# Kernel tuning notes

Hardware: AMD Instinct MI355X
Metric: run time of the kernel (lower is better)

Reference implementation:

```python
import jax, jax.numpy as jnp
import numpy as np

N = 50000          # num nodes
E = 1_000_000      # num edges (no self loops by construction)
IN_CH = 128        # in_channels
HEADS = 4
OUT_CH = 16        # out_channels per head
HID = HEADS * OUT_CH  # 64
NEG_SLOPE = 0.2


def setup_inputs() -> dict:
    key = jax.random.key(0)
    k1, k2, k3, k4, k5, k6 = jax.random.split(key, 6)
    x = jax.random.normal(k1, (N, IN_CH), jnp.float32)
    # edges with guaranteed row != col (so add_self_loops == plain concat)
    row = jax.random.randint(k2, (E,), 0, N, dtype=jnp.int32)
    off = jax.random.randint(k3, (E,), 1, N, dtype=jnp.int32)
    col = (row + off) % N
    edge_index = jnp.stack([row, col], axis=0)  # [2, E]
    # xavier-uniform linear weight [HID, IN_CH] (bias=False in module)
    lim_w = float(np.sqrt(6.0 / (IN_CH + HID)))
    W = jax.random.uniform(k4, (HID, IN_CH), jnp.float32, -lim_w, lim_w)
    # xavier-uniform attention vectors [HEADS, OUT_CH]
    lim_a = float(np.sqrt(6.0 / (HEADS + OUT_CH)))
    att_src = jax.random.uniform(k5, (HEADS, OUT_CH), jnp.float32, -lim_a, lim_a)
    att_dst = jax.random.uniform(k6, (HEADS, OUT_CH), jnp.float32, -lim_a, lim_a)
    bias = jnp.zeros((HID,), jnp.float32)
    return {"x": x, "edge_index": edge_index, "W": W,
            "att_src": att_src, "att_dst": att_dst, "bias": bias}


def reference(x, edge_index, W, att_src, att_dst, bias):
    # add self loops (input edges have no self loops, so this matches torch)
    loops = jnp.arange(N, dtype=edge_index.dtype)
    ei = jnp.concatenate([edge_index, jnp.stack([loops, loops], axis=0)], axis=1)
    row, col = ei[0], ei[1]                      # [E+N]
    proj = (x @ W.T).reshape(N, HEADS, OUT_CH)   # [N, H, C]
    src = proj[row]                              # [E+N, H, C] gather
    dst = proj[col]                              # [E+N, H, C] gather
    # MX attention logits per edge per head
    logits = (jnp.einsum('ehc,hc->eh', src, att_src)
              + jnp.einsum('ehc,hc->eh', dst, att_dst))
    logits = jax.nn.leaky_relu(logits, NEG_SLOPE)            # [E+N, H]
    # segment softmax over destination node (all heads at once)
    m = jax.ops.segment_max(logits, col, num_segments=N)    # [N, H]
    e = jnp.exp(logits - m[col])
    s = jax.ops.segment_sum(e, col, num_segments=N)         # [N, H]
    w = e / s[col]                                           # [E+N, H]
    # attention-weighted scatter-add aggregation
    out = jax.ops.segment_sum(src * w[..., None], col, num_segments=N)  # [N, H, C]
    return out.reshape(N, HID) + bias
```

## Files before the change

### kernel.cpp

```cpp
#include <hip/hip_runtime.h>

#define IN_CH   128
#define HEADS   4
#define OUT_CH  16
#define HID     64
#define NEG_SLOPE 0.2f
#define LOG2E   1.44269504088896340736f

#define LDA 136

#define RB      6
#define RSZ     64
#define NRANGE  1024
#define SEG     4096
#define RWIN    2048
#define CWIN    2048

typedef __attribute__((ext_vector_type(8))) short short8;
typedef __attribute__((ext_vector_type(4))) float float4v;

__device__ __forceinline__ unsigned short f2bf(float f) {
    unsigned int u = __float_as_uint(f);
    u += 0x7FFFu + ((u >> 16) & 1u);
    return (unsigned short)(u >> 16);
}
__device__ __forceinline__ float bf2f(unsigned short u) {
    return __uint_as_float(((unsigned int)u) << 16);
}
__device__ __forceinline__ void unpack2(unsigned int u, float& lo, float& hi) {
    lo = __uint_as_float(u << 16);
    hi = __uint_as_float(u & 0xffff0000u);
}

__global__ __launch_bounds__(256) void proj_kernel(
    const float* __restrict__ x,
    const float* __restrict__ W,
    const float* __restrict__ att_src,
    const float* __restrict__ att_dst,
    unsigned short* __restrict__ proj,
    float* __restrict__ asrc,
    float* __restrict__ adst,
    int* __restrict__ gcur,
    int n_nodes)
{
    __shared__ unsigned short As[64 * LDA];
    __shared__ unsigned short Bs[64 * LDA];

    const int tid = threadIdx.x;

    if (blockIdx.x == 0) {
        #pragma unroll
        for (int i = tid; i < NRANGE; i += 256) gcur[i] = i * RWIN;
    }

    const int n0 = blockIdx.x * 64;

    #pragma unroll
    for (int i = 0; i < 8; ++i) {
        int idx4 = i * 256 + tid;
        int row  = idx4 >> 5;
        int c4   = (idx4 & 31) * 4;
        float4 v = *(const float4*)(W + row * IN_CH + c4);
        ushort4 o;
        o.x = f2bf(v.x); o.y = f2bf(v.y); o.z = f2bf(v.z); o.w = f2bf(v.w);
        *(ushort4*)(&Bs[row * LDA + c4]) = o;
    }
    #pragma unroll
    for (int i = 0; i < 8; ++i) {
        int idx4 = i * 256 + tid;
        int row  = idx4 >> 5;
        int c4   = (idx4 & 31) * 4;
        int n    = n0 + row;
        float4 v = make_float4(0.f, 0.f, 0.f, 0.f);
        if (n < n_nodes) v = *(const float4*)(x + (size_t)n * IN_CH + c4);
        ushort4 o;
        o.x = f2bf(v.x); o.y = f2bf(v.y); o.z = f2bf(v.z); o.w = f2bf(v.w);
        *(ushort4*)(&As[row * LDA + c4]) = o;
    }
    __syncthreads();

    const int w    = tid >> 6;
    const int lane = tid & 63;
    const int l16  = lane & 15;
    const int quad = lane >> 4;

    float4v acc0 = {0.f,0.f,0.f,0.f};
    float4v acc1 = {0.f,0.f,0.f,0.f};
    float4v acc2 = {0.f,0.f,0.f,0.f};
    float4v acc3 = {0.f,0.f,0.f,0.f};

    const unsigned short* arow = &As[(w * 16 + l16) * LDA + quad * 8];
    const unsigned short* b0   = &Bs[( 0 + l16) * LDA + quad * 8];
    const unsigned short* b1   = &Bs[(16 + l16) * LDA + quad * 8];
    const unsigned short* b2   = &Bs[(32 + l16) * LDA + quad * 8];
    const unsigned short* b3   = &Bs[(48 + l16) * LDA + quad * 8];

    #pragma unroll
    for (int k0 = 0; k0 < IN_CH; k0 += 32) {
        short8 a  = *(const short8*)(arow + k0);
        acc0 = __builtin_amdgcn_mfma_f32_16x16x32_bf16(a, *(const short8*)(b0 + k0), acc0, 0, 0, 0);
        acc1 = __builtin_amdgcn_mfma_f32_16x16x32_bf16(a, *(const short8*)(b1 + k0), acc1, 0, 0, 0);
        acc2 = __builtin_amdgcn_mfma_f32_16x16x32_bf16(a, *(const short8*)(b2 + k0), acc2, 0, 0, 0);
        acc3 = __builtin_amdgcn_mfma_f32_16x16x32_bf16(a, *(const short8*)(b3 + k0), acc3, 0, 0, 0);
    }

    const float as0 = att_src[ 0 + l16], ad0 = att_dst[ 0 + l16];
    const float as1 = att_src[16 + l16], ad1 = att_dst[16 + l16];
    const float as2 = att_src[32 + l16], ad2 = att_dst[32 + l16];
    const float as3 = att_src[48 + l16], ad3 = att_dst[48 + l16];

    #pragma unroll
    for (int r = 0; r < 4; ++r) {
        const int n = n0 + w * 16 + quad * 4 + r;
        const bool ok = (n < n_nodes);
        float v0 = acc0[r], v1 = acc1[r], v2 = acc2[r], v3 = acc3[r];
        if (ok) {
            proj[(size_t)n * HID +  0 + l16] = f2bf(v0);
            proj[(size_t)n * HID + 16 + l16] = f2bf(v1);
            proj[(size_t)n * HID + 32 + l16] = f2bf(v2);
            proj[(size_t)n * HID + 48 + l16] = f2bf(v3);
        }
        float s0 = v0 * as0, s1 = v1 * as1, s2 = v2 * as2, s3 = v3 * as3;
        float d0 = v0 * ad0, d1 = v1 * ad1, d2 = v2 * ad2, d3 = v3 * ad3;
        #pragma unroll
        for (int off = 8; off >= 1; off >>= 1) {
            s0 += __shfl_down(s0, off, 16);
            s1 += __shfl_down(s1, off, 16);
            s2 += __shfl_down(s2, off, 16);
            s3 += __shfl_down(s3, off, 16);
            d0 += __shfl_down(d0, off, 16);
            d1 += __shfl_down(d1, off, 16);
            d2 += __shfl_down(d2, off, 16);
            d3 += __shfl_down(d3, off, 16);
        }
        if (ok && l16 == 0) {
            asrc[n * HEADS + 0] = s0 * LOG2E;
            asrc[n * HEADS + 1] = s1 * LOG2E;
            asrc[n * HEADS + 2] = s2 * LOG2E;
            asrc[n * HEADS + 3] = s3 * LOG2E;
            adst[n * HEADS + 0] = d0 * LOG2E;
            adst[n * HEADS + 1] = d1 * LOG2E;
            adst[n * HEADS + 2] = d2 * LOG2E;
            adst[n * HEADS + 3] = d3 * LOG2E;
        }
    }
}

__global__ __launch_bounds__(256) void bin_kernel(
    const int* __restrict__ src, const int* __restrict__ dst,
    int* __restrict__ gcur, unsigned int* __restrict__ ebuf, int n_edges)
{
    __shared__ unsigned int eb[SEG];
    __shared__ int lc[NRANGE];

    const int b = blockIdx.x;
    const int t = threadIdx.x;

    #pragma unroll
    for (int i = t; i < NRANGE; i += 256) lc[i] = 0;
    __syncthreads();

    const int e0  = b * SEG;
    const int e1  = min(e0 + SEG, n_edges);
    const int cnt = e1 - e0;

    for (int e = e0 + t * 4; e < e1; e += 1024) {
        if (e + 4 <= e1) {
            const int4 s4 = *(const int4*)(src + e);
            const int4 d4 = *(const int4*)(dst + e);
            {
                const int r = d4.x >> RB; atomicAdd(&lc[r], 1);
                eb[e - e0 + 0] = ((unsigned int)r << 22) | ((unsigned int)(d4.x & (RSZ - 1)) << 16) | (unsigned int)s4.x;
            }
            {
                const int r = d4.y >> RB; atomicAdd(&lc[r], 1);
                eb[e - e0 + 1] = ((unsigned int)r << 22) | ((unsigned int)(d4.y & (RSZ - 1)) << 16) | (unsigned int)s4.y;
            }
            {
                const int r = d4.z >> RB; atomicAdd(&lc[r], 1);
                eb[e - e0 + 2] = ((unsigned int)r << 22) | ((unsigned int)(d4.z & (RSZ - 1)) << 16) | (unsigned int)s4.z;
            }
            {
                const int r = d4.w >> RB; atomicAdd(&lc[r], 1);
                eb[e - e0 + 3] = ((unsigned int)r << 22) | ((unsigned int)(d4.w & (RSZ - 1)) << 16) | (unsigned int)s4.w;
            }
        } else {
            for (int q = e; q < e1; ++q) {
                const int d = dst[q];
                const int r = d >> RB;
                atomicAdd(&lc[r], 1);
                eb[q - e0] = ((unsigned int)r << 22) | ((unsigned int)(d & (RSZ - 1)) << 16) | (unsigned int)src[q];
            }
        }
    }
    __syncthreads();

    for (int r = t; r < NRANGE; r += 256) {
        const int c = lc[r];
        lc[r] = c ? atomicAdd(&gcur[r], c) : 0;
    }
    __syncthreads();

    for (int j = t; j < cnt; j += 256) {
        const unsigned int p = eb[j];
        const int slot = atomicAdd(&lc[p >> 22], 1);
        ebuf[slot] = p & 0x3FFFFFu;
    }
}

__global__ __launch_bounds__(256) void range_csr_kernel(
    const unsigned int* __restrict__ ebuf, const int* __restrict__ gcur,
    int2* __restrict__ rsdeg, unsigned short* __restrict__ csr, int n_nodes)
{
    __shared__ int hist[RSZ];
    __shared__ int cur[RSZ];

    const int r    = blockIdx.x;
    const int base = r << RB;
    const int lim  = min(RSZ, n_nodes - base);
    const int tid  = threadIdx.x;

    const int s0 = r * RWIN;
    const int s1 = gcur[r];

    if (tid < RSZ) hist[tid] = 0;
    __syncthreads();

    for (int j = s0 + tid; j < s1; j += 256)
        atomicAdd(&hist[ebuf[j] >> 16], 1);
    __syncthreads();

    if (tid < RSZ) {
        const int hv = hist[tid];
        int hc = hv;
        #pragma unroll
        for (int o = 1; o < 64; o <<= 1) {
            int u = __shfl_up(hc, o);
            if (tid >= o) hc += u;
        }
        const int start = r * CWIN + hc - hv;
        cur[tid] = start;
        if (tid < lim) rsdeg[base + tid] = make_int2(start, hv);
    }
    __syncthreads();

    for (int j = s0 + tid; j < s1; j += 256) {
        const unsigned int p = ebuf[j];
        const int slot = atomicAdd(&cur[p >> 16], 1);
        csr[slot] = (unsigned short)p;
    }
}

__global__ __launch_bounds__(256) void gather_kernel(
    const unsigned short* __restrict__ proj,
    const float* __restrict__ asrc,
    const float* __restrict__ adst,
    const int2* __restrict__ rsdeg,
    const unsigned short* __restrict__ csr,
    const float* __restrict__ bias,
    float* __restrict__ out,
    int n_nodes, int chunk)
{
    const int nb = (blockIdx.x & 7) * chunk + (blockIdx.x >> 3);
    const int l  = threadIdx.x & 63;
    const int w  = threadIdx.x >> 6;
    const int il = l & 7;
    const int g  = l >> 3;
    const int h  = il >> 1;
    const int ch = il * 8;

    int n = nb * 32 + w * 8 + g;
    const bool nok = (n < n_nodes);
    if (!nok) n = 0;

    const float  ad  = adst[n * HEADS + h];
    const float4 bv0 = *(const float4*)(bias + ch);
    const float4 bv1 = *(const float4*)(bias + ch + 4);

    float zs = asrc[n * HEADS + h] + ad;
    zs = fmaxf(zs, NEG_SLOPE * zs);
    float s = exp2f(zs);
    float a0, a1, a2, a3, a4, a5, a6, a7;
    {
        const uint4 ps = *(const uint4*)(proj + (size_t)n * HID + ch);
        float p0, p1, p2, p3, p4, p5, p6, p7;
        unpack2(ps.x, p0, p1); unpack2(ps.y, p2, p3);
        unpack2(ps.z, p4, p5); unpack2(ps.w, p6, p7);
        a0 = s * p0; a1 = s * p1; a2 = s * p2; a3 = s * p3;
        a4 = s * p4; a5 = s * p5; a6 = s * p6; a7 = s * p7;
    }

    const int2 rd   = rsdeg[n];
    const int start = rd.x;
    const int deg   = nok ? rd.y : 0;

    int m = deg;
    m = max(m, __shfl_xor(m, 8));
    m = max(m, __shfl_xor(m, 16));
    m = max(m, __shfl_xor(m, 32));
    const int kmax = __builtin_amdgcn_readfirstlane(m);

    #define STEP(K)                                                           \
    {                                                                         \
        const bool act = (K) < deg;                                           \
        int sid = (int)csr[start + (K)];   \
        sid = act ? sid : 0;                  \
        const uint4 pv = *(const uint4*)(proj + (size_t)sid * HID + ch);      \
        float av = asrc[sid * HEADS + h] + ad;                                \
        av = fmaxf(av, NEG_SLOPE * av);                                       \
        float e = exp2f(av);                                                  \
        e = act ? e : 0.f;                                                    \
        s += e;                                                               \
        float p0, p1, p2, p3, p4, p5, p6, p7;                                 \
        unpack2(pv.x, p0, p1); unpack2(pv.y, p2, p3);                         \
        unpack2(pv.z, p4, p5); unpack2(pv.w, p6, p7);                         \
        a0 = fmaf(e, p0, a0); a1 = fmaf(e, p1, a1);                           \
        a2 = fmaf(e, p2, a2); a3 = fmaf(e, p3, a3);                           \
        a4 = fmaf(e, p4, a4); a5 = fmaf(e, p5, a5);                           \
        a6 = fmaf(e, p6, a6); a7 = fmaf(e, p7, a7);                           \
    }

    for (int k = 0; k < kmax; k += 4) {
        STEP(k);
        STEP(k + 1);
        STEP(k + 2);
        STEP(k + 3);
    }
    #undef STEP

    if (nok) {
        const float inv = 1.0f / s;
        float4 o0, o1;
        o0.x = a0 * inv + bv0.x;
        o0.y = a1 * inv + bv0.y;
        o0.z = a2 * inv + bv0.z;
        o0.w = a3 * inv + bv0.w;
        o1.x = a4 * inv + bv1.x;
        o1.y = a5 * inv + bv1.y;
        o1.z = a6 * inv + bv1.z;
        o1.w = a7 * inv + bv1.w;
        *(float4*)(out + (size_t)n * HID + ch)     = o0;
        *(float4*)(out + (size_t)n * HID + ch + 4) = o1;
    }
}

static inline size_t align16(size_t o) { return (o + 15) & ~(size_t)15; }

extern "C" void kernel_launch(void* const* d_in, const int* in_sizes, int n_in,
                              void* d_out, int out_size, void* d_ws, size_t ws_size,
                              hipStream_t stream)
{
    const float* x       = (const float*)d_in[0];
    const int*   ei      = (const int*)d_in[1];
    const float* W       = (const float*)d_in[2];
    const float* att_src = (const float*)d_in[3];
    const float* att_dst = (const float*)d_in[4];
    const float* bias    = (const float*)d_in[5];
    float* out           = (float*)d_out;

    const int n_nodes = in_sizes[0] / IN_CH;
    const int n_edges = in_sizes[1] / 2;
    const int nblk    = (n_edges + SEG - 1) / SEG;
    const int nrange  = (n_nodes + RSZ - 1) / RSZ;
    const int nproj   = (n_nodes + 63) / 64;

    const int* src = ei;
    const int* dst = ei + n_edges;

    char* base = (char*)d_ws;
    size_t o = 0;
    unsigned short* proj = (unsigned short*)(base + o); o = align16(o + (size_t)n_nodes * HID * 2);
    float* asrc      = (float*)(base + o); o = align16(o + (size_t)n_nodes * HEADS * 4);
    float* adst      = (float*)(base + o); o = align16(o + (size_t)n_nodes * HEADS * 4);
    int2*  rsdeg     = (int2*)(base + o);  o = align16(o + (size_t)n_nodes * 8);
    unsigned short* csr = (unsigned short*)(base + o); o = align16(o + (size_t)NRANGE * CWIN * 2);
    unsigned int* ebuf = (unsigned int*)(base + o); o = align16(o + (size_t)NRANGE * RWIN * 4);
    int*   gcur      = (int*)(base + o);   o = align16(o + (size_t)NRANGE * 4);

    proj_kernel<<<nproj, 256, 0, stream>>>(
        x, W, att_src, att_dst, proj, asrc, adst, gcur, n_nodes);

    bin_kernel<<<nblk, 256, 0, stream>>>(src, dst, gcur, ebuf, n_edges);

    range_csr_kernel<<<nrange, 256, 0, stream>>>(ebuf, gcur, rsdeg, csr, n_nodes);

    const int nbk   = (n_nodes + 31) / 32;
    const int chunk = (nbk + 7) / 8;
    gather_kernel<<<chunk * 8, 256, 0, stream>>>(
        proj, asrc, adst, rsdeg, csr, bias, out, n_nodes, chunk);
}
```

Measured before the change: 133.0 us.

## Fuse projection with binning and build per-range CSR inside gather kernel

Merges the projection and edge-binning kernels into one launch, with separate block ranges doing each job, and folds the per-range CSR build into the gather kernel. The CSR now lives in shared memory, and gather blocks cover 64 nodes with 512 threads. This removes two kernel launches and the global CSR/rsdeg round trips. It also doubles the bin segment size, uses packed bf16 conversion instructions, and resets gcur with a memset. In exchange, the gather kernel has more shared-memory setup, and per-range edges are capped at RWIN, which silently drops edges if a range overflows.

```diff
diff --git a/kernel.cpp b/kernel.cpp
--- a/kernel.cpp
+++ b/kernel.cpp
@@ -12,9 +12,8 @@
 #define RB      6
 #define RSZ     64
 #define NRANGE  1024
-#define SEG     4096
+#define SEG     8192
 #define RWIN    2048
-#define CWIN    2048
 
 typedef __attribute__((ext_vector_type(8))) short short8;
 typedef __attribute__((ext_vector_type(4))) float float4v;
@@ -24,15 +23,17 @@
     u += 0x7FFFu + ((u >> 16) & 1u);
     return (unsigned short)(u >> 16);
 }
-__device__ __forceinline__ float bf2f(unsigned short u) {
-    return __uint_as_float(((unsigned int)u) << 16);
+__device__ __forceinline__ unsigned int cvt_pk_bf16(float lo, float hi) {
+    unsigned int r;
+    asm("v_cvt_pk_bf16_f32 %0, %1, %2" : "=v"(r) : "v"(lo), "v"(hi));
+    return r;
 }
 __device__ __forceinline__ void unpack2(unsigned int u, float& lo, float& hi) {
     lo = __uint_as_float(u << 16);
     hi = __uint_as_float(u & 0xffff0000u);
 }
 
-__global__ __launch_bounds__(256) void proj_kernel(
+__global__ __launch_bounds__(256) void proj_bin_kernel(
     const float* __restrict__ x,
     const float* __restrict__ W,
     const float* __restrict__ att_src,
@@ -40,18 +41,76 @@
     unsigned short* __restrict__ proj,
     float* __restrict__ asrc,
     float* __restrict__ adst,
+    const int* __restrict__ src,
+    const int* __restrict__ dst,
     int* __restrict__ gcur,
-    int n_nodes)
+    unsigned int* __restrict__ ebuf,
+    int n_nodes, int n_edges, int nblk_proj)
 {
-    __shared__ unsigned short As[64 * LDA];
-    __shared__ unsigned short Bs[64 * LDA];
+    __shared__ __align__(16) char smraw[SEG * 4 + NRANGE * 4];
 
     const int tid = threadIdx.x;
 
-    if (blockIdx.x == 0) {
+    if (blockIdx.x >= nblk_proj) {
+        unsigned int* eb = (unsigned int*)smraw;
+        int*          lc = (int*)(smraw + SEG * 4);
+
+        const int b = blockIdx.x - nblk_proj;
         #pragma unroll
-        for (int i = tid; i < NRANGE; i += 256) gcur[i] = i * RWIN;
-    }
+        for (int i = tid; i < NRANGE; i += 256) lc[i] = 0;
+        __syncthreads();
+
+        const int e0  = b * SEG;
+        const int e1  = min(e0 + SEG, n_edges);
+        const int cnt = e1 - e0;
+
+        for (int e = e0 + tid * 4; e < e1; e += 1024) {
+            if (e + 4 <= e1) {
+                const int4 s4 = *(const int4*)(src + e);
+                const int4 d4 = *(const int4*)(dst + e);
+                {
+                    const int r = d4.x >> RB; atomicAdd(&lc[r], 1);
+                    eb[e - e0 + 0] = ((unsigned int)r << 22) | ((unsigned int)(d4.x & (RSZ - 1)) << 16) | (unsigned int)s4.x;
+                }
+                {
+                    const int r = d4.y >> RB; atomicAdd(&lc[r], 1);
+                    eb[e - e0 + 1] = ((unsigned int)r << 22) | ((unsigned int)(d4.y & (RSZ - 1)) << 16) | (unsigned int)s4.y;
+                }
+                {
+                    const int r = d4.z >> RB; atomicAdd(&lc[r], 1);
+                    eb[e - e0 + 2] = ((unsigned int)r << 22) | ((unsigned int)(d4.z & (RSZ - 1)) << 16) | (unsigned int)s4.z;
+                }
+                {
+                    const int r = d4.w >> RB; atomicAdd(&lc[r], 1);
+                    eb[e - e0 + 3] = ((unsigned int)r << 22) | ((unsigned int)(d4.w & (RSZ - 1)) << 16) | (unsigned int)s4.w;
+                }
+            } else {
+                for (int q = e; q < e1; ++q) {
+                    const int d = dst[q];
+                    const int r = d >> RB;
+                    atomicAdd(&lc[r], 1);
+                    eb[q - e0] = ((unsigned int)r << 22) | ((unsigned int)(d & (RSZ - 1)) << 16) | (unsigned int)src[q];
+                }
+            }
+        }
+        __syncthreads();
+
+        for (int r = tid; r < NRANGE; r += 256) {
+            const int c = lc[r];
+            if (c) lc[r] = r * RWIN + atomicAdd(&gcur[r], c);
+        }
+        __syncthreads();
+
+        for (int j = tid; j < cnt; j += 256) {
+            const unsigned int p = eb[j];
+            const int slot = atomicAdd(&lc[p >> 22], 1);
+            ebuf[slot] = p & 0x3FFFFFu;
+        }
+        return;
+    }
+
+    unsigned short* As = (unsigned short*)smraw;
+    unsigned short* Bs = (unsigned short*)(smraw + 64 * LDA * 2);
 
     const int n0 = blockIdx.x * 64;
 
@@ -61,9 +120,10 @@
         int row  = idx4 >> 5;
         int c4   = (idx4 & 31) * 4;
         float4 v = *(const float4*)(W + row * IN_CH + c4);
-        ushort4 o;
-        o.x = f2bf(v.x); o.y = f2bf(v.y); o.z = f2bf(v.z); o.w = f2bf(v.w);
-        *(ushort4*)(&Bs[row * LDA + c4]) = o;
+        uint2 o;
+        o.x = cvt_pk_bf16(v.x, v.y);
+        o.y = cvt_pk_bf16(v.z, v.w);
+        *(uint2*)(&Bs[row * LDA + c4]) = o;
     }
     #pragma unroll
     for (int i = 0; i < 8; ++i) {
@@ -73,9 +133,10 @@
         int n    = n0 + row;
         float4 v = make_float4(0.f, 0.f, 0.f, 0.f);
         if (n < n_nodes) v = *(const float4*)(x + (size_t)n * IN_CH + c4);
-        ushort4 o;
-        o.x = f2bf(v.x); o.y = f2bf(v.y); o.z = f2bf(v.z); o.w = f2bf(v.w);
-        *(ushort4*)(&As[row * LDA + c4]) = o;
+        uint2 o;
+        o.x = cvt_pk_bf16(v.x, v.y);
+        o.y = cvt_pk_bf16(v.z, v.w);
+        *(uint2*)(&As[row * LDA + c4]) = o;
     }
     __syncthreads();
 
@@ -146,88 +207,37 @@
     }
 }
 
-__global__ __launch_bounds__(256) void bin_kernel(
-    const int* __restrict__ src, const int* __restrict__ dst,
-    int* __restrict__ gcur, unsigned int* __restrict__ ebuf, int n_edges)
+__global__ __launch_bounds__(512) void gather_kernel(
+    const unsigned short* __restrict__ proj,
+    const float* __restrict__ asrc,
+    const float* __restrict__ adst,
+    const int* __restrict__ gcur,
+    const unsigned int* __restrict__ ebuf,
+    const float* __restrict__ bias,
+    float* __restrict__ out,
+    int n_nodes)
 {
-    __shared__ unsigned int eb[SEG];
-    __shared__ int lc[NRANGE];
-
-    const int b = blockIdx.x;
-    const int t = threadIdx.x;
-
-    #pragma unroll
-    for (int i = t; i < NRANGE; i += 256) lc[i] = 0;
-    __syncthreads();
-
-    const int e0  = b * SEG;
-    const int e1  = min(e0 + SEG, n_edges);
-    const int cnt = e1 - e0;
-
-    for (int e = e0 + t * 4; e < e1; e += 1024) {
-        if (e + 4 <= e1) {
-            const int4 s4 = *(const int4*)(src + e);
-            const int4 d4 = *(const int4*)(dst + e);
-            {
-                const int r = d4.x >> RB; atomicAdd(&lc[r], 1);
-                eb[e - e0 + 0] = ((unsigned int)r << 22) | ((unsigned int)(d4.x & (RSZ - 1)) << 16) | (unsigned int)s4.x;
-            }
-            {
-                const int r = d4.y >> RB; atomicAdd(&lc[r], 1);
-                eb[e - e0 + 1] = ((unsigned int)r << 22) | ((unsigned int)(d4.y & (RSZ - 1)) << 16) | (unsigned int)s4.y;
-            }
-            {
-                const int r = d4.z >> RB; atomicAdd(&lc[r], 1);
-                eb[e - e0 + 2] = ((unsigned int)r << 22) | ((unsigned int)(d4.z & (RSZ - 1)) << 16) | (unsigned int)s4.z;
-            }
-            {
-                const int r = d4.w >> RB; atomicAdd(&lc[r], 1);
-                eb[e - e0 + 3] = ((unsigned int)r << 22) | ((unsigned int)(d4.w & (RSZ - 1)) << 16) | (unsigned int)s4.w;
-            }
-        } else {
-            for (int q = e; q < e1; ++q) {
-                const int d = dst[q];
-                const int r = d >> RB;
-                atomicAdd(&lc[r], 1);
-                eb[q - e0] = ((unsigned int)r << 22) | ((unsigned int)(d & (RSZ - 1)) << 16) | (unsigned int)src[q];
-            }
-        }
-    }
-    __syncthreads();
-
-    for (int r = t; r < NRANGE; r += 256) {
-        const int c = lc[r];
-        lc[r] = c ? atomicAdd(&gcur[r], c) : 0;
-    }
-    __syncthreads();
-
-    for (int j = t; j < cnt; j += 256) {
-        const unsigned int p = eb[j];
-        const int slot = atomicAdd(&lc[p >> 22], 1);
-        ebuf[slot] = p & 0x3FFFFFu;
-    }
-}
-
-__global__ __launch_bounds__(256) void range_csr_kernel(
-    const unsigned int* __restrict__ ebuf, const int* __restrict__ gcur,
-    int2* __restrict__ rsdeg, unsigned short* __restrict__ csr, int n_nodes)
-{
+    __shared__ unsigned short csr_s[RWIN + 128];
     __shared__ int hist[RSZ];
+    __shared__ int stt[RSZ];
     __shared__ int cur[RSZ];
 
     const int r    = blockIdx.x;
-    const int base = r << RB;
-    const int lim  = min(RSZ, n_nodes - base);
+    const int base = r * RSZ;
     const int tid  = threadIdx.x;
 
+    if (tid < RSZ) hist[tid] = 0;
+    __syncthreads();
+
+    const int total = min(gcur[r], RWIN);
     const int s0 = r * RWIN;
-    const int s1 = gcur[r];
-
-    if (tid < RSZ) hist[tid] = 0;
-    __syncthreads();
-
-    for (int j = s0 + tid; j < s1; j += 256)
-        atomicAdd(&hist[ebuf[j] >> 16], 1);
+
+    unsigned int ev0 = 0, ev1 = 0, ev2 = 0, ev3 = 0;
+    const int j0 = tid, j1 = tid + 512, j2 = tid + 1024, j3 = tid + 1536;
+    if (j0 < total) { ev0 = ebuf[s0 + j0]; atomicAdd(&hist[ev0 >> 16], 1); }
+    if (j1 < total) { ev1 = ebuf[s0 + j1]; atomicAdd(&hist[ev1 >> 16], 1); }
+    if (j2 < total) { ev2 = ebuf[s0 + j2]; atomicAdd(&hist[ev2 >> 16], 1); }
+    if (j3 < total) { ev3 = ebuf[s0 + j3]; atomicAdd(&hist[ev3 >> 16], 1); }
     __syncthreads();
 
     if (tid < RSZ) {
@@ -238,38 +248,26 @@
             int u = __shfl_up(hc, o);
             if (tid >= o) hc += u;
         }
-        const int start = r * CWIN + hc - hv;
-        cur[tid] = start;
-        if (tid < lim) rsdeg[base + tid] = make_int2(start, hv);
-    }
-    __syncthreads();
-
-    for (int j = s0 + tid; j < s1; j += 256) {
-        const unsigned int p = ebuf[j];
-        const int slot = atomicAdd(&cur[p >> 16], 1);
-        csr[slot] = (unsigned short)p;
-    }
-}
-
-__global__ __launch_bounds__(256) void gather_kernel(
-    const unsigned short* __restrict__ proj,
-    const float* __restrict__ asrc,
-    const float* __restrict__ adst,
-    const int2* __restrict__ rsdeg,
-    const unsigned short* __restrict__ csr,
-    const float* __restrict__ bias,
-    float* __restrict__ out,
-    int n_nodes, int chunk)
-{
-    const int nb = (blockIdx.x & 7) * chunk + (blockIdx.x >> 3);
-    const int l  = threadIdx.x & 63;
-    const int w  = threadIdx.x >> 6;
+        stt[tid] = hc - hv;
+        cur[tid] = hc - hv;
+    }
+    __syncthreads();
+
+    if (j0 < total) { const int sl = atomicAdd(&cur[ev0 >> 16], 1); csr_s[sl] = (unsigned short)ev0; }
+    if (j1 < total) { const int sl = atomicAdd(&cur[ev1 >> 16], 1); csr_s[sl] = (unsigned short)ev1; }
+    if (j2 < total) { const int sl = atomicAdd(&cur[ev2 >> 16], 1); csr_s[sl] = (unsigned short)ev2; }
+    if (j3 < total) { const int sl = atomicAdd(&cur[ev3 >> 16], 1); csr_s[sl] = (unsigned short)ev3; }
+    __syncthreads();
+
+    const int l  = tid & 63;
+    const int w  = tid >> 6;
     const int il = l & 7;
     const int g  = l >> 3;
     const int h  = il >> 1;
     const int ch = il * 8;
 
-    int n = nb * 32 + w * 8 + g;
+    const int nd = w * 8 + g;
+    int n = base + nd;
     const bool nok = (n < n_nodes);
     if (!nok) n = 0;
 
@@ -290,9 +288,8 @@
         a4 = s * p4; a5 = s * p5; a6 = s * p6; a7 = s * p7;
     }
 
-    const int2 rd   = rsdeg[n];
-    const int start = rd.x;
-    const int deg   = nok ? rd.y : 0;
+    const int st  = stt[nd];
+    const int deg = nok ? hist[nd] : 0;
 
     int m = deg;
     m = max(m, __shfl_xor(m, 8));
@@ -303,7 +300,7 @@
     #define STEP(K)                                                           \
     {                                                                         \
         const bool act = (K) < deg;                                           \
-        int sid = (int)csr[start + (K)];   \
+        int sid = (int)csr_s[st + (K)];       \
         sid = act ? sid : 0;                  \
         const uint4 pv = *(const uint4*)(proj + (size_t)sid * HID + ch);      \
         float av = asrc[sid * HEADS + h] + ad;                                \
@@ -360,9 +357,9 @@
 
     const int n_nodes = in_sizes[0] / IN_CH;
     const int n_edges = in_sizes[1] / 2;
-    const int nblk    = (n_edges + SEG - 1) / SEG;
+    const int nproj   = (n_nodes + 63) / 64;
+    const int nbin    = (n_edges + SEG - 1) / SEG;
     const int nrange  = (n_nodes + RSZ - 1) / RSZ;
-    const int nproj   = (n_nodes + 63) / 64;
 
     const int* src = ei;
     const int* dst = ei + n_edges;
@@ -372,20 +369,15 @@
     unsigned short* proj = (unsigned short*)(base + o); o = align16(o + (size_t)n_nodes * HID * 2);
     float* asrc      = (float*)(base + o); o = align16(o + (size_t)n_nodes * HEADS * 4);
     float* adst      = (float*)(base + o); o = align16(o + (size_t)n_nodes * HEADS * 4);
-    int2*  rsdeg     = (int2*)(base + o);  o = align16(o + (size_t)n_nodes * 8);
-    unsigned short* csr = (unsigned short*)(base + o); o = align16(o + (size_t)NRANGE * CWIN * 2);
-    unsigned int* ebuf = (unsigned int*)(base + o); o = align16(o + (size_t)NRANGE * RWIN * 4);
+    unsigned int* ebuf = (unsigned int*)(base + o); o = align16(o + (size_t)nrange * RWIN * 4);
     int*   gcur      = (int*)(base + o);   o = align16(o + (size_t)NRANGE * 4);
 
-    proj_kernel<<<nproj, 256, 0, stream>>>(
-        x, W, att_src, att_dst, proj, asrc, adst, gcur, n_nodes);
-
-    bin_kernel<<<nblk, 256, 0, stream>>>(src, dst, gcur, ebuf, n_edges);
-
-    range_csr_kernel<<<nrange, 256, 0, stream>>>(ebuf, gcur, rsdeg, csr, n_nodes);
-
-    const int nbk   = (n_nodes + 31) / 32;
-    const int chunk = (nbk + 7) / 8;
-    gather_kernel<<<chunk * 8, 256, 0, stream>>>(
-        proj, asrc, adst, rsdeg, csr, bias, out, n_nodes, chunk);
-}
+    hipMemsetAsync(gcur, 0, (size_t)NRANGE * 4, stream);
+
+    proj_bin_kernel<<<nproj + nbin, 256, 0, stream>>>(
+        x, W, att_src, att_dst, proj, asrc, adst,
+        src, dst, gcur, ebuf, n_nodes, n_edges, nproj);
+
+    gather_kernel<<<nrange, 512, 0, stream>>>(
+        proj, asrc, adst, gcur, ebuf, bias, out, n_nodes);
+}
```

Result: no change. 131.8 us (-1.0%).
